# Kernel optimization log

Measured on AMD Instinct MI355X. Metric: run time of the kernel, lower is better.

Reference implementation:

```python
import jax, jax.numpy as jnp
import numpy as np

H, D = 16, 64            # heads_num, mouse_hidden_dim // heads_num
START_FRAME = 9728       # current_start (token units)
GLOBAL_END_PREV = 9728   # kv_cache['global_end_index'] before this call
LOCAL_END_PREV = 9728    # kv_cache['local_end_index'] before this call
SINK = 0                 # sink_tokens in source
WINDOW = 8192            # max_attention_size = local_attn_size (token units)


def _rope_interleaved(x, cos_h, sin_h):
    # non-neox (interleaved) rotary: x [B,S,H,D], cos_h/sin_h [S, D//2]
    x1 = x[..., 0::2]
    x2 = x[..., 1::2]
    c = cos_h[None, :, None, :]
    s = sin_h[None, :, None, :]
    o1 = x1 * c - x2 * s
    o2 = x2 * c + x1 * s
    return jnp.stack([o1, o2], axis=-1).reshape(x.shape)


def setup_inputs() -> dict:
    key = jax.random.key(0)
    ks = jax.random.split(key, 7)
    B, S, C = 1, 1024, 10240
    return {
        'q': jax.random.normal(ks[0], (B, S, H, D), jnp.float32),
        'k': jax.random.normal(ks[1], (B, S, H, D), jnp.float32),
        'v': jax.random.normal(ks[2], (B, S, H, D), jnp.float32),
        'cache_k': jax.random.normal(ks[3], (B, C, H, D), jnp.float32),
        'cache_v': jax.random.normal(ks[4], (B, C, H, D), jnp.float32),
        'freqs_cos': jax.random.uniform(ks[5], (START_FRAME + S, D), jnp.float32, -1.0, 1.0),
        'freqs_sin': jax.random.uniform(ks[6], (START_FRAME + S, D), jnp.float32, -1.0, 1.0),
    }


def reference(q, k, v, cache_k, cache_v, freqs_cos, freqs_sin):
    B, S, _, _ = q.shape
    # _apply_rotary_emb_qk: slice freqs at start_offset, take every-other col (cos_half)
    cos_h = freqs_cos[START_FRAME:START_FRAME + S, ::2]  # [S, D//2]
    sin_h = freqs_sin[START_FRAME:START_FRAME + S, ::2]
    q_r = _rope_interleaved(q, cos_h, sin_h)
    k_r = _rope_interleaved(k, cos_h, sin_h)

    # ring-buffer KV-cache update (all index math is static Python ints)
    current_end = START_FRAME + S
    cache_size = cache_k.shape[1]
    num_new = S
    if current_end > GLOBAL_END_PREV and num_new + LOCAL_END_PREV > cache_size:
        num_evicted = num_new + LOCAL_END_PREV - cache_size
        num_rolled = LOCAL_END_PREV - num_evicted - SINK
        rolled_k = jax.lax.dynamic_slice_in_dim(cache_k, SINK + num_evicted, num_rolled, axis=1)
        rolled_v = jax.lax.dynamic_slice_in_dim(cache_v, SINK + num_evicted, num_rolled, axis=1)
        cache_k = cache_k.at[:, SINK:SINK + num_rolled].set(rolled_k)
        cache_v = cache_v.at[:, SINK:SINK + num_rolled].set(rolled_v)
        local_end = LOCAL_END_PREV + current_end - GLOBAL_END_PREV - num_evicted
    else:
        local_end = LOCAL_END_PREV + current_end - GLOBAL_END_PREV
    local_start = local_end - num_new
    cache_k = cache_k.at[:, local_start:local_end].set(k_r)
    cache_v = cache_v.at[:, local_start:local_end].set(v)

    # windowed (last local_attn_size tokens) non-causal attention
    cache_start = max(0, local_end - WINDOW)
    wk = cache_k[:, cache_start:local_end]  # [B, W, H, D]
    wv = cache_v[:, cache_start:local_end]
    scale = 1.0 / np.float32(np.sqrt(D))
    scores = jnp.einsum('bqhd,bkhd->bhqk', q_r, wk) * scale
    probs = jax.nn.softmax(scores, axis=-1)
    out = jnp.einsum('bhqk,bkhd->bqhd', probs, wv)
    return out.reshape(B, S, H * D)
```

## Files before the change

### kernel.cpp

```cpp
#include <hip/hip_runtime.h>

#define HH 16
#define DD 64
#define SQ 1024
#define LW 8192
#define OLDK 7168
#define CACHE_BASE 2560
#define SFRAME 9728
#define KSPLIT 8
#define KPER (LW / KSPLIT)
#define NSTEP (KPER / 64)

#define KB_OFF 0u
#define VT_OFF 16777216u
#define QB_OFF 33554432u
#define OP_OFF 35651584u
#define LP_OFF 69206016u

typedef __bf16 bf16x8 __attribute__((ext_vector_type(8)));
typedef float floatx16 __attribute__((ext_vector_type(16)));
typedef unsigned uintx2 __attribute__((ext_vector_type(2)));
typedef unsigned uintx4 __attribute__((ext_vector_type(4)));

__device__ __forceinline__ unsigned short f2bf(float f) {
  unsigned u = __builtin_bit_cast(unsigned, f);
  u += 0x7fffu + ((u >> 16) & 1u);
  return (unsigned short)(u >> 16);
}

__device__ __forceinline__ float fast_exp2(float x) {
#if __has_builtin(__builtin_amdgcn_exp2f)
  return __builtin_amdgcn_exp2f(x);
#else
  return __builtin_exp2f(x);
#endif
}

__device__ __forceinline__ unsigned pack_bf2(float a, float b) {
#if __has_builtin(__builtin_amdgcn_cvt_pk_bf16_f32)
  typedef __bf16 bf16x2_t __attribute__((ext_vector_type(2)));
  bf16x2_t r = __builtin_amdgcn_cvt_pk_bf16_f32(a, b);
  return __builtin_bit_cast(unsigned, r);
#else
  unsigned ua = __builtin_bit_cast(unsigned, a) + 0x8000u;
  unsigned ub = __builtin_bit_cast(unsigned, b) + 0x8000u;
  return __builtin_amdgcn_perm(ub, ua, 0x07060302);
#endif
}

__device__ __forceinline__ void async16(void* lds, const void* g) {
  __builtin_amdgcn_global_load_lds((__attribute__((address_space(1))) void*)(g),
                                   (__attribute__((address_space(3))) void*)(lds),
                                   16, 0, 0);
}

__global__ __launch_bounds__(256) void prepass(
    const float* __restrict__ qin, const float* __restrict__ kin,
    const float* __restrict__ vin, const float* __restrict__ ck,
    const float* __restrict__ cv, const float* __restrict__ fc,
    const float* __restrict__ fs, unsigned short* __restrict__ Kb,
    unsigned short* __restrict__ Vt, unsigned short* __restrict__ Qb) {
  int b = blockIdx.x, t = threadIdx.x;
  if (b < 1024) {
    __shared__ float tl[128 * 64];
    int h = b >> 6, kk0 = (b & 63) * 128;
    int c = t & 15;
#pragma unroll
    for (int it = 0; it < 8; it++) {
      int kk = it * 16 + (t >> 4);
      int gk = kk0 + kk;
      const float* src = (gk < OLDK)
                             ? cv + (CACHE_BASE + gk) * (HH * DD) + h * DD + 4 * c
                             : vin + (gk - OLDK) * (HH * DD) + h * DD + 4 * c;
      float4 vv = *(const float4*)src;
      int cg = c ^ (kk >> 3);
      *(float4*)(tl + kk * 64 + cg * 4) = vv;
    }
    __syncthreads();
    int kq = t & 15;
#pragma unroll
    for (int jt = 0; jt < 4; jt++) {
      int d = jt * 16 + (t >> 4);
      ushort4 lo, hi;
      unsigned short tmp[8];
#pragma unroll
      for (int j = 0; j < 8; j++) {
        int kk = 8 * kq + j;
        int cg = (d >> 2) ^ kq;
        tmp[j] = f2bf(tl[kk * 64 + cg * 4 + (d & 3)]);
      }
      lo.x = tmp[0]; lo.y = tmp[1]; lo.z = tmp[2]; lo.w = tmp[3];
      hi.x = tmp[4]; hi.y = tmp[5]; hi.z = tmp[6]; hi.w = tmp[7];
      unsigned short* dst = Vt + (h * DD + d) * LW + kk0 + 8 * kq;
      *(ushort4*)(dst) = lo;
      *(ushort4*)(dst + 4) = hi;
    }
  } else if (b < 8192) {
    int b1 = b - 1024;
    int h = b1 / 448, g = b1 % 448;
    int kk = g * 16 + (t >> 4);
    int lane = t & 15;
    float4 val = *(const float4*)(ck + (CACHE_BASE + kk) * (HH * DD) + h * DD + lane * 4);
    ushort4 o;
    o.x = f2bf(val.x); o.y = f2bf(val.y); o.z = f2bf(val.z); o.w = f2bf(val.w);
    *(ushort4*)(Kb + (h * LW + kk) * DD + lane * 4) = o;
  } else if (b < 10240) {
    int b2 = b - 8192;
    int rh = b2 * 8 + (t >> 5);
    int s = rh >> 4, h = rh & 15, i = t & 31;
    float2 x = *(const float2*)(kin + s * (HH * DD) + h * DD + 2 * i);
    float c = fc[(SFRAME + s) * DD + 2 * i];
    float sn = fs[(SFRAME + s) * DD + 2 * i];
    ushort2 o;
    o.x = f2bf(x.x * c - x.y * sn);
    o.y = f2bf(x.y * c + x.x * sn);
    *(ushort2*)(Kb + (h * LW + OLDK + s) * DD + 2 * i) = o;
  } else {
    int b3 = b - 10240;
    int rh = b3 * 8 + (t >> 5);
    int s = rh >> 4, h = rh & 15, i = t & 31;
    const float SC = 0.18033688011112042f;
    float2 x = *(const float2*)(qin + s * (HH * DD) + h * DD + 2 * i);
    float c = fc[(SFRAME + s) * DD + 2 * i];
    float sn = fs[(SFRAME + s) * DD + 2 * i];
    ushort2 o;
    o.x = f2bf((x.x * c - x.y * sn) * SC);
    o.y = f2bf((x.y * c + x.x * sn) * SC);
    *(ushort2*)(Qb + (h * SQ + s) * DD + 2 * i) = o;
  }
}

__global__ __launch_bounds__(256, 2) void attn(
    const unsigned short* __restrict__ Kb, const unsigned short* __restrict__ Vt,
    const unsigned short* __restrict__ Qb, float* __restrict__ Op,
    float* __restrict__ Lp) {
  __shared__ __align__(16) unsigned char sK[2][8192];
  __shared__ __align__(16) unsigned char sV[2][8192];

  int bid = blockIdx.x;
  int g = bid & 127, qb = bid >> 7;
  int h = g & 15, ks = g >> 4;
  int t = threadIdx.x;
  int w = t >> 6, lane = t & 63;
  int l31 = lane & 31, e = lane >> 5;
  int q0 = qb * 256 + w * 64;

  int baseA = (l31 & 7) ^ ((l31 >> 3) & 7);
  int baseB = (l31 & 7) ^ (((l31 >> 3) + 4) & 7);

  bf16x8 qf[2][4];
#pragma unroll
  for (int tq = 0; tq < 2; tq++) {
    const unsigned short* qptr = Qb + (h * SQ + q0 + 32 * tq + l31) * DD + 8 * e;
#pragma unroll
    for (int c = 0; c < 4; c++) qf[tq][c] = *(const bf16x8*)(qptr + 16 * c);
  }

  floatx16 o[2][2];
#pragma unroll
  for (int a = 0; a < 2; a++)
#pragma unroll
    for (int bb = 0; bb < 2; bb++)
#pragma unroll
      for (int i = 0; i < 16; i++) o[a][bb][i] = 0.f;
  float ls[2] = {0.f, 0.f};

  const unsigned short* KbH = Kb + h * (LW * DD);
  const unsigned short* VtH = Vt + h * (DD * LW);
  int kkBase = ks * KPER;

  auto stage = [&](int buf, int kk0) {
#pragma unroll
    for (int hf = 0; hf < 2; hf++) {
      int gi = w * 128 + hf * 64 + lane;
      int rr = gi >> 3;
      int src = (gi & 7) ^ (rr & 7) ^ ((rr >> 3) & 7);
      async16(sK[buf] + gi * 16, KbH + (kk0 + rr) * DD + src * 8);
      async16(sV[buf] + gi * 16, VtH + rr * LW + kk0 + src * 8);
    }
  };

  stage(0, kkBase);

  for (int st = 0; st < NSTEP; st++) {
    __syncthreads();
    if (st + 1 < NSTEP) stage((st + 1) & 1, kkBase + (st + 1) * 64);
    const unsigned char* cK = sK[st & 1];
    const unsigned char* cV = sV[st & 1];

    floatx16 s[2][2];
#pragma unroll
    for (int a = 0; a < 2; a++)
#pragma unroll
      for (int bb = 0; bb < 2; bb++)
#pragma unroll
        for (int i = 0; i < 16; i++) s[a][bb][i] = 0.f;
#pragma unroll
    for (int c = 0; c < 4; c++) {
      int pA = (2 * c + e) ^ baseA;
      int pB = (2 * c + e) ^ baseB;
      bf16x8 ka = *(const bf16x8*)(cK + (l31 * 8 + pA) * 16);
      bf16x8 kb = *(const bf16x8*)(cK + ((l31 + 32) * 8 + pB) * 16);
      s[0][0] = __builtin_amdgcn_mfma_f32_32x32x16_bf16(ka, qf[0][c], s[0][0], 0, 0, 0);
      s[0][1] = __builtin_amdgcn_mfma_f32_32x32x16_bf16(kb, qf[0][c], s[0][1], 0, 0, 0);
      s[1][0] = __builtin_amdgcn_mfma_f32_32x32x16_bf16(ka, qf[1][c], s[1][0], 0, 0, 0);
      s[1][1] = __builtin_amdgcn_mfma_f32_32x32x16_bf16(kb, qf[1][c], s[1][1], 0, 0, 0);
    }

    unsigned pk[2][2][4][2];
#pragma unroll
    for (int tq = 0; tq < 2; tq++) {
#pragma unroll
      for (int tk = 0; tk < 2; tk++) {
#pragma unroll
        for (int i = 0; i < 16; i++) s[tq][tk][i] = fast_exp2(s[tq][tk][i]);
        float ps = 0.f;
#pragma unroll
        for (int i = 0; i < 16; i++) ps += s[tq][tk][i];
        ls[tq] += ps;
#pragma unroll
        for (int bq = 0; bq < 4; bq++)
#pragma unroll
          for (int p = 0; p < 2; p++)
            pk[tq][tk][bq][p] = pack_bf2(s[tq][tk][4 * bq + 2 * p], s[tq][tk][4 * bq + 2 * p + 1]);
      }
    }

    bf16x8 pf[2][4];
#pragma unroll
    for (int tq = 0; tq < 2; tq++) {
#pragma unroll
      for (int tk = 0; tk < 2; tk++) {
#pragma unroll
        for (int kcp = 0; kcp < 2; kcp++) {
          uintx2 r0 = __builtin_amdgcn_permlane32_swap(pk[tq][tk][2 * kcp][0],
                                                       pk[tq][tk][2 * kcp + 1][0], false, false);
          uintx2 r1 = __builtin_amdgcn_permlane32_swap(pk[tq][tk][2 * kcp][1],
                                                       pk[tq][tk][2 * kcp + 1][1], false, false);
          uintx4 f;
          f[0] = r0[0]; f[1] = r1[0]; f[2] = r0[1]; f[3] = r1[1];
          pf[tq][2 * tk + kcp] = __builtin_bit_cast(bf16x8, f);
        }
      }
    }

#pragma unroll
    for (int kc = 0; kc < 4; kc++) {
      int pA = (2 * kc + e) ^ baseA;
      int pB = (2 * kc + e) ^ baseB;
      bf16x8 va = *(const bf16x8*)(cV + (l31 * 8 + pA) * 16);
      bf16x8 vb = *(const bf16x8*)(cV + ((l31 + 32) * 8 + pB) * 16);
      o[0][0] = __builtin_amdgcn_mfma_f32_32x32x16_bf16(va, pf[0][kc], o[0][0], 0, 0, 0);
      o[0][1] = __builtin_amdgcn_mfma_f32_32x32x16_bf16(vb, pf[0][kc], o[0][1], 0, 0, 0);
      o[1][0] = __builtin_amdgcn_mfma_f32_32x32x16_bf16(va, pf[1][kc], o[1][0], 0, 0, 0);
      o[1][1] = __builtin_amdgcn_mfma_f32_32x32x16_bf16(vb, pf[1][kc], o[1][1], 0, 0, 0);
    }
  }

#pragma unroll
  for (int tq = 0; tq < 2; tq++) {
    float l = ls[tq];
    l += __shfl_xor(l, 32, 64);
    int qrow = q0 + 32 * tq + l31;
    float* op = Op + (((ks * 16 + h) * SQ) + qrow) * DD;
#pragma unroll
    for (int t4 = 0; t4 < 4; t4++) {
      float4 a, b;
      a.x = o[tq][0][4 * t4 + 0]; a.y = o[tq][0][4 * t4 + 1];
      a.z = o[tq][0][4 * t4 + 2]; a.w = o[tq][0][4 * t4 + 3];
      b.x = o[tq][1][4 * t4 + 0]; b.y = o[tq][1][4 * t4 + 1];
      b.z = o[tq][1][4 * t4 + 2]; b.w = o[tq][1][4 * t4 + 3];
      *(float4*)(op + 8 * t4 + 4 * e) = a;
      *(float4*)(op + 32 + 8 * t4 + 4 * e) = b;
    }
    if (e == 0) Lp[(ks * 16 + h) * SQ + qrow] = l;
  }
}

__global__ __launch_bounds__(256) void combine(const float* __restrict__ Op,
                                               const float* __restrict__ Lp,
                                               float* __restrict__ out) {
  int idx = blockIdx.x * 256 + threadIdx.x;
  int d = idx & 63, q = (idx >> 6) & 1023, h = idx >> 16;
  float num = 0.f, den = 0.f;
#pragma unroll
  for (int s = 0; s < KSPLIT; s++) {
    int row = (s * 16 + h) * SQ + q;
    num += Op[row * DD + d];
    den += Lp[row];
  }
  out[q * (HH * DD) + h * DD + d] = num / den;
}

extern "C" void kernel_launch(void* const* d_in, const int* in_sizes, int n_in,
                              void* d_out, int out_size, void* d_ws, size_t ws_size,
                              hipStream_t stream) {
  const float* q  = (const float*)d_in[0];
  const float* k  = (const float*)d_in[1];
  const float* v  = (const float*)d_in[2];
  const float* ck = (const float*)d_in[3];
  const float* cv = (const float*)d_in[4];
  const float* fc = (const float*)d_in[5];
  const float* fs = (const float*)d_in[6];
  float* out = (float*)d_out;
  char* ws = (char*)d_ws;

  unsigned short* Kb = (unsigned short*)(ws + KB_OFF);
  unsigned short* Vt = (unsigned short*)(ws + VT_OFF);
  unsigned short* Qb = (unsigned short*)(ws + QB_OFF);
  float* Op = (float*)(ws + OP_OFF);
  float* Lp = (float*)(ws + LP_OFF);

  prepass<<<12288, 256, 0, stream>>>(q, k, v, ck, cv, fc, fs, Kb, Vt, Qb);
  attn<<<512, 256, 0, stream>>>(Kb, Vt, Qb, Op, Lp);
  combine<<<4096, 256, 0, stream>>>(Op, Lp, out);
}
```

Measured before the change: 188.6 us.

## Double attention key split, store bf16 partials, vectorize combine

Raises the key-dimension split from 8 to 16, so the attention grid grows to 1024 blocks, and raises the occupancy hint in launch bounds from 2 to 4 blocks per CU. The aim is to fill the CUs better and hide memory latency. Per-split partial outputs are now written as packed bf16 instead of fp32, which keeps partial traffic about the same despite twice as many splits. The combine kernel now reads 4 values per thread and multiplies by a reciprocal. The costs are possible register spills under the tighter launch bound, lower-precision partial sums, and more combine reads per output.

```diff
diff --git a/kernel.cpp b/kernel.cpp
--- a/kernel.cpp
+++ b/kernel.cpp
@@ -7,7 +7,7 @@
 #define OLDK 7168
 #define CACHE_BASE 2560
 #define SFRAME 9728
-#define KSPLIT 8
+#define KSPLIT 16
 #define KPER (LW / KSPLIT)
 #define NSTEP (KPER / 64)
 
@@ -130,15 +130,15 @@
   }
 }
 
-__global__ __launch_bounds__(256, 2) void attn(
+__global__ __launch_bounds__(256, 4) void attn(
     const unsigned short* __restrict__ Kb, const unsigned short* __restrict__ Vt,
-    const unsigned short* __restrict__ Qb, float* __restrict__ Op,
+    const unsigned short* __restrict__ Qb, unsigned short* __restrict__ Op,
     float* __restrict__ Lp) {
   __shared__ __align__(16) unsigned char sK[2][8192];
   __shared__ __align__(16) unsigned char sV[2][8192];
 
   int bid = blockIdx.x;
-  int g = bid & 127, qb = bid >> 7;
+  int g = bid & 255, qb = bid >> 8;
   int h = g & 15, ks = g >> 4;
   int t = threadIdx.x;
   int w = t >> 6, lane = t & 63;
@@ -262,34 +262,42 @@
     float l = ls[tq];
     l += __shfl_xor(l, 32, 64);
     int qrow = q0 + 32 * tq + l31;
-    float* op = Op + (((ks * 16 + h) * SQ) + qrow) * DD;
+    unsigned short* op = Op + (((ks * 16 + h) * SQ) + qrow) * DD;
 #pragma unroll
     for (int t4 = 0; t4 < 4; t4++) {
-      float4 a, b;
-      a.x = o[tq][0][4 * t4 + 0]; a.y = o[tq][0][4 * t4 + 1];
-      a.z = o[tq][0][4 * t4 + 2]; a.w = o[tq][0][4 * t4 + 3];
-      b.x = o[tq][1][4 * t4 + 0]; b.y = o[tq][1][4 * t4 + 1];
-      b.z = o[tq][1][4 * t4 + 2]; b.w = o[tq][1][4 * t4 + 3];
-      *(float4*)(op + 8 * t4 + 4 * e) = a;
-      *(float4*)(op + 32 + 8 * t4 + 4 * e) = b;
+      uint2 a, b;
+      a.x = pack_bf2(o[tq][0][4 * t4 + 0], o[tq][0][4 * t4 + 1]);
+      a.y = pack_bf2(o[tq][0][4 * t4 + 2], o[tq][0][4 * t4 + 3]);
+      b.x = pack_bf2(o[tq][1][4 * t4 + 0], o[tq][1][4 * t4 + 1]);
+      b.y = pack_bf2(o[tq][1][4 * t4 + 2], o[tq][1][4 * t4 + 3]);
+      *(uint2*)(op + 8 * t4 + 4 * e) = a;
+      *(uint2*)(op + 32 + 8 * t4 + 4 * e) = b;
     }
     if (e == 0) Lp[(ks * 16 + h) * SQ + qrow] = l;
   }
 }
 
-__global__ __launch_bounds__(256) void combine(const float* __restrict__ Op,
+__global__ __launch_bounds__(256) void combine(const unsigned short* __restrict__ Op,
                                                const float* __restrict__ Lp,
                                                float* __restrict__ out) {
   int idx = blockIdx.x * 256 + threadIdx.x;
-  int d = idx & 63, q = (idx >> 6) & 1023, h = idx >> 16;
-  float num = 0.f, den = 0.f;
+  int d4 = idx & 15, q = (idx >> 4) & 1023, h = idx >> 14;
+  float num[4] = {0.f, 0.f, 0.f, 0.f};
+  float den = 0.f;
 #pragma unroll
   for (int s = 0; s < KSPLIT; s++) {
     int row = (s * 16 + h) * SQ + q;
-    num += Op[row * DD + d];
+    uint2 pkv = *(const uint2*)(Op + row * DD + 4 * d4);
+    num[0] += __builtin_bit_cast(float, pkv.x << 16);
+    num[1] += __builtin_bit_cast(float, pkv.x & 0xffff0000u);
+    num[2] += __builtin_bit_cast(float, pkv.y << 16);
+    num[3] += __builtin_bit_cast(float, pkv.y & 0xffff0000u);
     den += Lp[row];
   }
-  out[q * (HH * DD) + h * DD + d] = num / den;
+  float r = 1.0f / den;
+  float4 ov;
+  ov.x = num[0] * r; ov.y = num[1] * r; ov.z = num[2] * r; ov.w = num[3] * r;
+  *(float4*)(out + q * (HH * DD) + h * DD + 4 * d4) = ov;
 }
 
 extern "C" void kernel_launch(void* const* d_in, const int* in_sizes, int n_in,
@@ -308,10 +316,10 @@
   unsigned short* Kb = (unsigned short*)(ws + KB_OFF);
   unsigned short* Vt = (unsigned short*)(ws + VT_OFF);
   unsigned short* Qb = (unsigned short*)(ws + QB_OFF);
-  float* Op = (float*)(ws + OP_OFF);
+  unsigned short* Op = (unsigned short*)(ws + OP_OFF);
   float* Lp = (float*)(ws + LP_OFF);
 
   prepass<<<12288, 256, 0, stream>>>(q, k, v, ck, cv, fc, fs, Kb, Vt, Qb);
-  attn<<<512, 256, 0, stream>>>(Kb, Vt, Qb, Op, Lp);
-  combine<<<4096, 256, 0, stream>>>(Op, Lp, out);
-}
+  attn<<<1024, 256, 0, stream>>>(Kb, Vt, Qb, Op, Lp);
+  combine<<<1024, 256, 0, stream>>>(Op, Lp, out);
+}
```

Result: slower. 689.4 us (+265.5%).
